# Optimization experiments

Measured on AMD Instinct MI355X. Metric: run time of the kernel, lower is better.

Reference implementation:

```python
import jax, jax.numpy as jnp
import numpy as np

B, XL, YL, D = 16, 2048, 2048, 1024

def setup_inputs() -> dict:
    key = jax.random.key(0)
    kx, ky, km, kw = jax.random.split(key, 4)
    x = jax.random.normal(kx, (B, XL, D), dtype=jnp.float32)
    y = jax.random.normal(ky, (B, YL, D), dtype=jnp.float32)
    # True == padding position (masked with -inf in the torch module)
    y_mask = jax.random.randint(km, (B, YL), 0, 2).astype(bool)
    # shared projection Linear(embed_dim, embed_dim); scale ~ 1/sqrt(D)
    W = jax.random.normal(kw, (D, D), dtype=jnp.float32) * (1.0 / np.sqrt(D))
    b = jnp.zeros((D,), dtype=jnp.float32)
    return {"x": x, "y": y, "y_mask": y_mask, "W": W, "b": b}

def reference(x, y, y_mask, W, b):
    # shared ReLU(Linear) projection applied to both x and y
    x_proj = jax.nn.relu(jnp.einsum('bxd,ed->bxe', x, W) + b)   # (B, XL, D)
    y_proj = jax.nn.relu(jnp.einsum('byd,ed->bye', y, W) + b)   # (B, YL, D)
    scores = jnp.einsum('bxd,byd->bxy', x_proj, y_proj)          # (B, XL, YL)
    scores = jnp.where(y_mask[:, None, :], -jnp.inf, scores)
    weights = jax.nn.softmax(scores, axis=2)
    contexts = jnp.einsum('bxy,byd->bxd', weights, y)            # (B, XL, D)
    return contexts
```

## Files before the change

kernel.cpp:

```cpp
#include <hip/hip_runtime.h>
#include <math.h>
#include <stdint.h>


typedef __attribute__((ext_vector_type(8))) _Float16 f16x8;
typedef __attribute__((ext_vector_type(4))) float f32x4;

__device__ __forceinline__ ushort h2u(_Float16 h) { return __builtin_bit_cast(ushort, h); }

__device__ __forceinline__ void ld16(const ushort* g, ushort* l) {
    __builtin_amdgcn_global_load_lds(
        (__attribute__((address_space(1))) void*)(g),
        (__attribute__((address_space(3))) void*)(l), 16, 0, 0);
}

#define BAR()   { __builtin_amdgcn_s_barrier(); asm volatile("" ::: "memory"); }
#define LGKM0() { asm volatile("s_waitcnt lgkmcnt(0)" ::: "memory"); __builtin_amdgcn_sched_barrier(0); }
#define VMW(N)  asm volatile("s_waitcnt vmcnt(" #N ")" ::: "memory");

template<int EPI, int MODE>
__global__ __launch_bounds__(512) void gemm256(
    const ushort* __restrict__ A, size_t zsA,
    const ushort* __restrict__ B, size_t zsB,
    const float* __restrict__ bias, const int* __restrict__ nyBuf,
    float* __restrict__ Cf, ushort* __restrict__ Chi, size_t zsC,
    int sdA, int sdB, int N, int T)
{
    __shared__ char ldsb[131072];

    const int gx = gridDim.x, gxy = gx * gridDim.y;
    const int total = gxy * gridDim.z;
    int hsw = blockIdx.z * gxy + blockIdx.y * gx + blockIdx.x;
    hsw = (hsw & 7) * (total >> 3) + (hsw >> 3);
    const int z = hsw / gxy;
    const int rem = hsw - z * gxy;
    const int by = rem / gx;
    const int bx = rem - by * gx;

    int NY = 0, NYPAD = 0;
    if constexpr (MODE != 0) { NY = nyBuf[2 * z]; NYPAD = nyBuf[2 * z + 1]; }
    if constexpr (MODE == 1) { if (by * 256 >= 2048 && by * 256 - 2048 >= NYPAD) return; }
    if constexpr (MODE == 2) { if (bx * 256 >= NYPAD) return; }
    if constexpr (MODE == 3) { T = NYPAD >> 6; }

    const int tid = threadIdx.x;
    const int lane = tid & 63;
    const int wv = tid >> 6, wm = wv >> 2, wn = wv & 3;
    const int m0 = by * 256, n0 = bx * 256;

    const int pl  = tid >> 3;
    const int ss  = (tid & 7) ^ (pl & 7);
    const int sr0 = 2 * pl + (ss >> 2);
    const int ske = (ss & 3) * 8;
    const int tb  = tid * 16;

    const ushort* gA0 = A + (size_t)z * zsA + (size_t)(m0 + sr0) * sdA + ske;
    const ushort* gA1 = A + (size_t)z * zsA + (size_t)(m0 + 128 + sr0) * sdA + ske;
    const ushort* gB0 = B + (size_t)z * zsB + (size_t)(n0 + sr0) * sdB + ske;
    const ushort* gB1 = B + (size_t)z * zsB + (size_t)(n0 + 128 + sr0) * sdB + ske;

#define ST_A(KOF, DOF) { ld16(gA0 + (KOF), (ushort*)(ldsb + (DOF) + tb));          \
                         ld16(gA1 + (KOF), (ushort*)(ldsb + (DOF) + 8192 + tb)); }
#define ST_B(KOF, DOF) { ld16(gB0 + (KOF), (ushort*)(ldsb + 65536 + (DOF) + tb));  \
                         ld16(gB1 + (KOF), (ushort*)(ldsb + 65536 + (DOF) + 8192 + tb)); }

    const int fr = lane & 15, fq = lane >> 4;
    const int sl = (((fr & 1) << 2) | fq) ^ ((fr >> 1) & 7);
    const int aoff = (wm * 64 + (fr >> 1)) * 128 + sl * 16;
    const int boff = (wn * 32 + (fr >> 1)) * 128 + sl * 16;

    f32x4 acc[8][4];
    #pragma unroll
    for (int i = 0; i < 8; ++i)
        #pragma unroll
        for (int j = 0; j < 4; ++j)
            acc[i][j] = (f32x4){0.f, 0.f, 0.f, 0.f};

    f16x8 a[4], b[4];

#define RD_B(DOF) { const char* p_ = ldsb + 65536 + (DOF) + boff;                  \
    b[0] = *(const f16x8*)(p_);        b[1] = *(const f16x8*)(p_ + 1024);          \
    b[2] = *(const f16x8*)(p_ + 2048); b[3] = *(const f16x8*)(p_ + 3072); }
#define RD_AL(DOF) { const char* p_ = ldsb + (DOF) + aoff;                         \
    a[0] = *(const f16x8*)(p_);        a[1] = *(const f16x8*)(p_ + 1024);          \
    a[2] = *(const f16x8*)(p_ + 2048); a[3] = *(const f16x8*)(p_ + 3072); }
#define RD_AH(DOF) { const char* p_ = ldsb + (DOF) + aoff + 4096;                  \
    a[0] = *(const f16x8*)(p_);        a[1] = *(const f16x8*)(p_ + 1024);          \
    a[2] = *(const f16x8*)(p_ + 2048); a[3] = *(const f16x8*)(p_ + 3072); }
#define MF_L { __builtin_amdgcn_s_setprio(1);                                      \
    _Pragma("unroll") for (int m_ = 0; m_ < 4; ++m_)                               \
        _Pragma("unroll") for (int n_ = 0; n_ < 4; ++n_)                           \
            acc[m_][n_] = __builtin_amdgcn_mfma_f32_16x16x32_f16(a[m_], b[n_], acc[m_][n_], 0, 0, 0); \
    __builtin_amdgcn_s_setprio(0); }
#define MF_H { __builtin_amdgcn_s_setprio(1);                                      \
    _Pragma("unroll") for (int m_ = 0; m_ < 4; ++m_)                               \
        _Pragma("unroll") for (int n_ = 0; n_ < 4; ++n_)                           \
            acc[m_ + 4][n_] = __builtin_amdgcn_mfma_f32_16x16x32_f16(a[m_], b[n_], acc[m_ + 4][n_], 0, 0, 0); \
    __builtin_amdgcn_s_setprio(0); }

#define TILE(BUF, S0, S1, S2, S3, W1, W3)                                          \
    RD_B((BUF)*32768); RD_AL((BUF)*32768);                                         \
    S0; BAR(); LGKM0(); MF_L; BAR();                                               \
    RD_AH((BUF)*32768);                                                            \
    S1; BAR(); LGKM0(); MF_H; W1; BAR();                                           \
    RD_B((BUF)*32768 + 16384); RD_AL((BUF)*32768 + 16384);                         \
    S2; BAR(); LGKM0(); MF_L; BAR();                                               \
    RD_AH((BUF)*32768 + 16384);                                                    \
    S3; BAR(); LGKM0(); MF_H; W3; BAR();

    ST_A(0, 0);      ST_B(0, 0);
    ST_A(32, 16384); ST_B(32, 16384);
    ST_A(64, 32768); ST_B(64, 32768);
    VMW(8);
    BAR();

    for (int it = 0; it < (T - 2) / 2; ++it) {
        TILE(0, ST_A(96, 49152),  ST_B(96, 49152),  ST_A(128, 0),     ST_B(128, 0),     VMW(8), VMW(8))
        TILE(1, ST_A(160, 16384), ST_B(160, 16384), ST_A(192, 32768), ST_B(192, 32768), VMW(8), VMW(8))
        gA0 += 128; gA1 += 128; gB0 += 128; gB1 += 128;
    }
    TILE(0, ST_A(96, 49152), ST_B(96, 49152), , , VMW(8), VMW(4))
    TILE(1, , , , , VMW(0), )

    #pragma unroll
    for (int n = 0; n < 4; ++n) {
        const int col = n0 + wn * 64 + n * 16 + fr;
        float bb = 0.f;
        if constexpr (EPI == 1) bb = bias[col];
        #pragma unroll
        for (int m = 0; m < 8; ++m) {
            const int row = m0 + wm * 128 + m * 16 + fq * 4;
            #pragma unroll
            for (int r = 0; r < 4; ++r) {
                const float v = acc[m][n][r];
                const size_t idx = (size_t)z * zsC + (size_t)(row + r) * N + col;
                if constexpr (EPI == 0) {
                    Cf[idx] = v;
                } else if constexpr (EPI == 1) {
                    Chi[idx] = h2u((_Float16)fmaxf(v + bb, 0.f));
                } else {
                    Cf[idx] = (col >= NY) ? -INFINITY : v;
                }
            }
        }
    }
#undef ST_A
#undef ST_B
#undef RD_B
#undef RD_AL
#undef RD_AH
#undef MF_L
#undef MF_H
#undef TILE
}

__global__ __launch_bounds__(256) void build_idx(const int* __restrict__ mask,
    int* __restrict__ idx, int* __restrict__ nyBuf)
{
    const int z = blockIdx.x;
    const int* mb = mask + (size_t)z * 2048;
    __shared__ int part[256];
    const int tid = threadIdx.x;
    int keep[8]; int c = 0;
    #pragma unroll
    for (int k = 0; k < 8; ++k) { keep[k] = (mb[tid * 8 + k] == 0); c += keep[k]; }
    part[tid] = c;
    for (int off = 1; off < 256; off <<= 1) {
        __syncthreads();
        const int v = (tid >= off) ? part[tid - off] : 0;
        __syncthreads();
        part[tid] += v;
    }
    __syncthreads();
    int pos = part[tid] - c;
    #pragma unroll
    for (int k = 0; k < 8; ++k)
        if (keep[k]) idx[(size_t)z * 2048 + (pos++)] = tid * 8 + k;
    if (tid == 255) {
        const int ny = part[255];
        int nyp = (ny + 255) & ~255;
        if (nyp < 256) nyp = 256;
        nyBuf[2 * z] = ny;
        nyBuf[2 * z + 1] = nyp;
    }
}

__global__ __launch_bounds__(256) void cvt_f16(const float* __restrict__ in,
    ushort* __restrict__ o, size_t sIn4, size_t sOut)
{
    const size_t z = blockIdx.z;
    const int i = blockIdx.x * 256 + threadIdx.x;
    const float4 v = reinterpret_cast<const float4*>(in)[z * sIn4 + i];
    ushort4 h;
    h.x = h2u((_Float16)v.x); h.y = h2u((_Float16)v.y);
    h.z = h2u((_Float16)v.z); h.w = h2u((_Float16)v.w);
    reinterpret_cast<ushort4*>(o + z * sOut)[i] = h;
}

__global__ __launch_bounds__(256) void gather_y(const float* __restrict__ y,
    const int* __restrict__ idx, const int* __restrict__ nyBuf,
    ushort* __restrict__ rH, ushort* __restrict__ tT,
    size_t sIn, size_t sR, size_t sT)
{
    __shared__ float tile[32][33];
    const size_t z = blockIdx.z;
    const int NY = nyBuf[2 * z], NYPAD = nyBuf[2 * z + 1];
    const int r0 = blockIdx.y * 32;
    if (r0 >= NYPAD) return;
    const int c0 = blockIdx.x * 32;
    const float* yb = y + z * sIn;
    const int* idxb = idx + z * 2048;
    const int tx = threadIdx.x & 31, ty = threadIdx.x >> 5;
    #pragma unroll
    for (int k = 0; k < 4; ++k) {
        const int i = r0 + ty + k * 8;
        float v = 0.f;
        if (i < NY) v = yb[(size_t)idxb[i] * 1024 + c0 + tx];
        tile[ty + k * 8][tx] = v;
        rH[z * sR + (size_t)i * 1024 + c0 + tx] = h2u((_Float16)v);
    }
    __syncthreads();
    #pragma unroll
    for (int k = 0; k < 4; ++k) {
        const int c = c0 + ty + k * 8;
        tT[z * sT + (size_t)c * 2048 + r0 + tx] = h2u((_Float16)tile[tx][ty + k * 8]);
    }
}

__global__ __launch_bounds__(256) void softmax_f16(const float* __restrict__ S,
    ushort* __restrict__ Wout, const int* __restrict__ nyBuf, size_t sS, size_t sW)
{
    const size_t row = blockIdx.x;
    const size_t b = row >> 11, r = row & 2047;
    const int nf4 = nyBuf[2 * b + 1] >> 2;
    const float4* p4 = reinterpret_cast<const float4*>(S + b * sS + r * 2048);
    ushort4* q4 = reinterpret_cast<ushort4*>(Wout + b * sW + r * 2048);
    const int tid = threadIdx.x;

    const float4 NEG = {-INFINITY, -INFINITY, -INFINITY, -INFINITY};
    float4 v0 = (tid < nf4) ? p4[tid] : NEG;
    float4 v1 = (tid + 256 < nf4) ? p4[tid + 256] : NEG;
    float m = fmaxf(fmaxf(fmaxf(v0.x, v0.y), fmaxf(v0.z, v0.w)),
                    fmaxf(fmaxf(v1.x, v1.y), fmaxf(v1.z, v1.w)));
    #pragma unroll
    for (int off = 32; off >= 1; off >>= 1)
        m = fmaxf(m, __shfl_xor(m, off));

    __shared__ float redm[4], reds[4];
    if ((tid & 63) == 0) redm[tid >> 6] = m;
    __syncthreads();
    m = fmaxf(fmaxf(redm[0], redm[1]), fmaxf(redm[2], redm[3]));

    float e[8];
    e[0] = __expf(v0.x - m); e[1] = __expf(v0.y - m);
    e[2] = __expf(v0.z - m); e[3] = __expf(v0.w - m);
    e[4] = __expf(v1.x - m); e[5] = __expf(v1.y - m);
    e[6] = __expf(v1.z - m); e[7] = __expf(v1.w - m);
    float s = ((e[0] + e[1]) + (e[2] + e[3])) + ((e[4] + e[5]) + (e[6] + e[7]));
    #pragma unroll
    for (int off = 32; off >= 1; off >>= 1)
        s += __shfl_xor(s, off);
    if ((tid & 63) == 0) reds[tid >> 6] = s;
    __syncthreads();
    s = reds[0] + reds[1] + reds[2] + reds[3];

    const float inv = 1.f / s;
    ushort4 o0, o1;
    o0.x = h2u((_Float16)(e[0] * inv)); o0.y = h2u((_Float16)(e[1] * inv));
    o0.z = h2u((_Float16)(e[2] * inv)); o0.w = h2u((_Float16)(e[3] * inv));
    o1.x = h2u((_Float16)(e[4] * inv)); o1.y = h2u((_Float16)(e[5] * inv));
    o1.z = h2u((_Float16)(e[6] * inv)); o1.w = h2u((_Float16)(e[7] * inv));
    if (tid < nf4) q4[tid] = o0;
    if (tid + 256 < nf4) q4[tid + 256] = o1;
}

extern "C" void kernel_launch(void* const* d_in, const int* in_sizes, int n_in,
                              void* d_out, int out_size, void* d_ws, size_t ws_size,
                              hipStream_t stream)
{
    const float* x    = (const float*)d_in[0];
    const float* y    = (const float*)d_in[1];
    const int* ymask  = (const int*)d_in[2];
    const float* W    = (const float*)d_in[3];
    const float* bias = (const float*)d_in[4];
    float* out = (float*)d_out;

    const size_t BD = 2097152;

    const size_t perBatch = 29360128ull;
    int G = 16;
    while (G > 1 && 4194304ull + (size_t)G * perBatch > ws_size) G >>= 1;

    uint8_t* wsb = (uint8_t*)d_ws;
    ushort* W16  = (ushort*)wsb;
    int* idxBuf  = (int*)(wsb + 2097152);
    int* nyBuf   = (int*)(wsb + 2097152 + 131072);
    uint8_t* r1  = wsb + 4194304;
    uint8_t* r2  = r1 + (size_t)G * 16777216;
    uint8_t* r3  = r2 + (size_t)G * 8388608;

    ushort* xyHi = (ushort*)r1;
    float*  sc   = (float*)r1;
    ushort* pHi  = (ushort*)r2;
    ushort* yT   = (ushort*)r3;

    cvt_f16<<<dim3(1024, 1, 1), dim3(256), 0, stream>>>(W, W16, 0, 0);
    build_idx<<<dim3(16), dim3(256), 0, stream>>>(ymask, idxBuf, nyBuf);

    for (int bs = 0; bs < 16; bs += G) {
        const float* xg = x + (size_t)bs * BD;
        const float* yg = y + (size_t)bs * BD;
        const int* nyB  = nyBuf + 2 * bs;

        cvt_f16<<<dim3(2048, 1, G), dim3(256), 0, stream>>>(
            xg, xyHi, BD / 4, 8388608);
        gather_y<<<dim3(32, 64, G), dim3(256), 0, stream>>>(
            yg, idxBuf + (size_t)bs * 2048, nyB,
            xyHi + BD, yT, BD, 8388608, BD);

        gemm256<1, 1><<<dim3(4, 16, G), dim3(512), 0, stream>>>(
            xyHi, 8388608, W16, 0,
            bias, nyB,
            nullptr, pHi, 4194304, 1024, 1024, 1024, 16);

        gemm256<2, 2><<<dim3(8, 8, G), dim3(512), 0, stream>>>(
            pHi, 4194304, pHi + BD, 4194304,
            nullptr, nyB,
            sc, nullptr, 4194304, 1024, 1024, 2048, 16);

        softmax_f16<<<dim3(G * 2048), dim3(256), 0, stream>>>(
            sc, pHi, nyB, 4194304, 4194304);

        gemm256<0, 3><<<dim3(4, 8, G), dim3(512), 0, stream>>>(
            pHi, 4194304, yT, 2097152,
            nullptr, nyB,
            out + (size_t)bs * BD, nullptr, BD, 2048, 2048, 1024, 32);
    }
}
```

Baseline: 512.6 us.

## Double-buffer LDS fragment registers to overlap reads with MFMA in GEMM

Splits the A/B fragment registers into two register sets so LDS reads for the next sub-tile are issued before the current MFMA block. Partial lgkmcnt waits replace full drains, and vmcnt thresholds are adjusted to match. It also rounds the padded valid-key count to 128 instead of 256, which could reduce wasted work on masked columns. The cost is higher register pressure, and the padding change may not fit a 256-wide GEMM tile.

```diff
diff --git a/kernel.cpp b/kernel.cpp
--- a/kernel.cpp
+++ b/kernel.cpp
@@ -14,9 +14,9 @@
         (__attribute__((address_space(3))) void*)(l), 16, 0, 0);
 }
 
-#define BAR()   { __builtin_amdgcn_s_barrier(); asm volatile("" ::: "memory"); }
-#define LGKM0() { asm volatile("s_waitcnt lgkmcnt(0)" ::: "memory"); __builtin_amdgcn_sched_barrier(0); }
-#define VMW(N)  asm volatile("s_waitcnt vmcnt(" #N ")" ::: "memory");
+#define BAR()  { __builtin_amdgcn_s_barrier(); asm volatile("" ::: "memory"); }
+#define VMW(N) asm volatile("s_waitcnt vmcnt(" #N ")" ::: "memory");
+#define LG(N)  { asm volatile("s_waitcnt lgkmcnt(" #N ")" ::: "memory"); __builtin_amdgcn_sched_barrier(0); }
 
 template<int EPI, int MODE>
 __global__ __launch_bounds__(512) void gemm256(
@@ -76,51 +76,51 @@
         for (int j = 0; j < 4; ++j)
             acc[i][j] = (f32x4){0.f, 0.f, 0.f, 0.f};
 
-    f16x8 a[4], b[4];
-
-#define RD_B(DOF) { const char* p_ = ldsb + 65536 + (DOF) + boff;                  \
-    b[0] = *(const f16x8*)(p_);        b[1] = *(const f16x8*)(p_ + 1024);          \
-    b[2] = *(const f16x8*)(p_ + 2048); b[3] = *(const f16x8*)(p_ + 3072); }
-#define RD_AL(DOF) { const char* p_ = ldsb + (DOF) + aoff;                         \
-    a[0] = *(const f16x8*)(p_);        a[1] = *(const f16x8*)(p_ + 1024);          \
-    a[2] = *(const f16x8*)(p_ + 2048); a[3] = *(const f16x8*)(p_ + 3072); }
-#define RD_AH(DOF) { const char* p_ = ldsb + (DOF) + aoff + 4096;                  \
-    a[0] = *(const f16x8*)(p_);        a[1] = *(const f16x8*)(p_ + 1024);          \
-    a[2] = *(const f16x8*)(p_ + 2048); a[3] = *(const f16x8*)(p_ + 3072); }
-#define MF_L { __builtin_amdgcn_s_setprio(1);                                      \
+    f16x8 a0[4], a1[4], bb0[4], bb1[4];
+
+#define RD4(DST, BASE) { const char* p_ = (BASE);                                  \
+    DST[0] = *(const f16x8*)(p_);        DST[1] = *(const f16x8*)(p_ + 1024);      \
+    DST[2] = *(const f16x8*)(p_ + 2048); DST[3] = *(const f16x8*)(p_ + 3072); }
+#define MFL(AV, BV) { __builtin_amdgcn_s_setprio(1);                               \
     _Pragma("unroll") for (int m_ = 0; m_ < 4; ++m_)                               \
         _Pragma("unroll") for (int n_ = 0; n_ < 4; ++n_)                           \
-            acc[m_][n_] = __builtin_amdgcn_mfma_f32_16x16x32_f16(a[m_], b[n_], acc[m_][n_], 0, 0, 0); \
+            acc[m_][n_] = __builtin_amdgcn_mfma_f32_16x16x32_f16(AV[m_], BV[n_], acc[m_][n_], 0, 0, 0); \
     __builtin_amdgcn_s_setprio(0); }
-#define MF_H { __builtin_amdgcn_s_setprio(1);                                      \
+#define MFH(AV, BV) { __builtin_amdgcn_s_setprio(1);                               \
     _Pragma("unroll") for (int m_ = 0; m_ < 4; ++m_)                               \
         _Pragma("unroll") for (int n_ = 0; n_ < 4; ++n_)                           \
-            acc[m_ + 4][n_] = __builtin_amdgcn_mfma_f32_16x16x32_f16(a[m_], b[n_], acc[m_ + 4][n_], 0, 0, 0); \
+            acc[m_ + 4][n_] = __builtin_amdgcn_mfma_f32_16x16x32_f16(AV[m_], BV[n_], acc[m_ + 4][n_], 0, 0, 0); \
     __builtin_amdgcn_s_setprio(0); }
 
-#define TILE(BUF, S0, S1, S2, S3, W1, W3)                                          \
-    RD_B((BUF)*32768); RD_AL((BUF)*32768);                                         \
-    S0; BAR(); LGKM0(); MF_L; BAR();                                               \
-    RD_AH((BUF)*32768);                                                            \
-    S1; BAR(); LGKM0(); MF_H; W1; BAR();                                           \
-    RD_B((BUF)*32768 + 16384); RD_AL((BUF)*32768 + 16384);                         \
-    S2; BAR(); LGKM0(); MF_L; BAR();                                               \
-    RD_AH((BUF)*32768 + 16384);                                                    \
-    S3; BAR(); LGKM0(); MF_H; W3; BAR();
+#define TILE(D0, D1, DN, S0, S1, S2, S3, V0, V2)                                   \
+    RD4(a1, ldsb + (D0) + aoff + 4096);                                            \
+    S0; BAR(); LG(4); MFL(a0, bb0); V0; BAR();                                     \
+    RD4(bb1, ldsb + 65536 + (D1) + boff); RD4(a0, ldsb + (D1) + aoff);             \
+    S1; BAR(); LG(8); MFH(a1, bb0); BAR();                                         \
+    RD4(a1, ldsb + (D1) + aoff + 4096);                                            \
+    S2; BAR(); LG(4); MFL(a0, bb1); V2; BAR();                                     \
+    RD4(bb0, ldsb + 65536 + (DN) + boff); RD4(a0, ldsb + (DN) + aoff);             \
+    S3; BAR(); LG(8); MFH(a1, bb1); BAR();
 
     ST_A(0, 0);      ST_B(0, 0);
     ST_A(32, 16384); ST_B(32, 16384);
     ST_A(64, 32768); ST_B(64, 32768);
     VMW(8);
     BAR();
+    RD4(bb0, ldsb + 65536 + boff);
+    RD4(a0, ldsb + aoff);
 
     for (int it = 0; it < (T - 2) / 2; ++it) {
-        TILE(0, ST_A(96, 49152),  ST_B(96, 49152),  ST_A(128, 0),     ST_B(128, 0),     VMW(8), VMW(8))
-        TILE(1, ST_A(160, 16384), ST_B(160, 16384), ST_A(192, 32768), ST_B(192, 32768), VMW(8), VMW(8))
+        TILE(0, 16384, 32768,
+             ST_A(96, 49152), ST_B(96, 49152), ST_A(128, 0), ST_B(128, 0),
+             VMW(6), VMW(6))
+        TILE(32768, 49152, 0,
+             ST_A(160, 16384), ST_B(160, 16384), ST_A(192, 32768), ST_B(192, 32768),
+             VMW(6), VMW(6))
         gA0 += 128; gA1 += 128; gB0 += 128; gB1 += 128;
     }
-    TILE(0, ST_A(96, 49152), ST_B(96, 49152), , , VMW(8), VMW(4))
-    TILE(1, , , , , VMW(0), )
+    TILE(0, 16384, 32768, ST_A(96, 49152), ST_B(96, 49152), , , VMW(6), VMW(4))
+    TILE(32768, 49152, 32768, , , , , VMW(0), )
 
     #pragma unroll
     for (int n = 0; n < 4; ++n) {
@@ -146,11 +146,9 @@
     }
 #undef ST_A
 #undef ST_B
-#undef RD_B
-#undef RD_AL
-#undef RD_AH
-#undef MF_L
-#undef MF_H
+#undef RD4
+#undef MFL
+#undef MFH
 #undef TILE
 }
 
@@ -178,7 +176,7 @@
         if (keep[k]) idx[(size_t)z * 2048 + (pos++)] = tid * 8 + k;
     if (tid == 255) {
         const int ny = part[255];
-        int nyp = (ny + 255) & ~255;
+        int nyp = (ny + 127) & ~127;
         if (nyp < 256) nyp = 256;
         nyBuf[2 * z] = ny;
         nyBuf[2 * z + 1] = nyp;
```

Measured after the change: 503.4 us. About the same (-1.8%).
